# Optimization experiments

Hardware: AMD Instinct MI355X
Metric: run time of the kernel (lower is better)

## Reference

```python
import jax, jax.numpy as jnp
import numpy as np

B, T, M = 32, 14, 2048
Q_DIM, KV_DIM, H = 768, 1024, 12
HD = Q_DIM // H
FF = 4 * Q_DIM
EPS = 1e-5


def layer_norm(x, g, b):
    mu = jnp.mean(x, axis=-1, keepdims=True)
    var = jnp.var(x, axis=-1, keepdims=True)
    return (x - mu) / jnp.sqrt(var + EPS) * g + b


def setup_inputs() -> dict:
    key = jax.random.key(0)
    ks = jax.random.split(key, 12)
    s = 0.02
    return {
        "expert_tokens": jax.random.normal(ks[0], (B, T, Q_DIM), jnp.float32),
        "key_value_embeddings": jax.random.normal(ks[1], (B, M, KV_DIM), jnp.float32),
        # per-expert-token query projections (stacked W_Q_list)
        "WQ": jax.random.normal(ks[2], (T, Q_DIM, Q_DIM), jnp.float32) * s,
        "bQ": jnp.zeros((T, Q_DIM), jnp.float32),
        "WK": jax.random.normal(ks[3], (KV_DIM, Q_DIM), jnp.float32) * s,
        "bK": jnp.zeros((Q_DIM,), jnp.float32),
        "WV": jax.random.normal(ks[4], (KV_DIM, Q_DIM), jnp.float32) * s,
        "bV": jnp.zeros((Q_DIM,), jnp.float32),
        "W1": jax.random.normal(ks[5], (Q_DIM, FF), jnp.float32) * s,
        "b1": jnp.zeros((FF,), jnp.float32),
        "W2": jax.random.normal(ks[6], (FF, Q_DIM), jnp.float32) * s,
        "b2": jnp.zeros((Q_DIM,), jnp.float32),
        "g1": jnp.ones((Q_DIM,), jnp.float32),
        "be1": jnp.zeros((Q_DIM,), jnp.float32),
        "g2": jnp.ones((Q_DIM,), jnp.float32),
        "be2": jnp.zeros((Q_DIM,), jnp.float32),
    }


def reference(expert_tokens, key_value_embeddings, WQ, bQ, WK, bK, WV, bV,
              W1, b1, W2, b2, g1, be1, g2, be2):
    b_, t_, e_ = expert_tokens.shape
    m_ = key_value_embeddings.shape[1]
    # Batched grouped projection: distinct W_Q per expert token (replaces the python loop)
    Q = (jnp.einsum('bte,teq->btq', expert_tokens, WQ) + bQ).reshape(b_, t_, H, HD)
    K = (key_value_embeddings @ WK + bK).reshape(b_, m_, H, HD)
    V = (key_value_embeddings @ WV + bV).reshape(b_, m_, H, HD)
    scale = jnp.sqrt(jnp.asarray(HD, jnp.float32))
    scores = jnp.einsum('bthd,bmhd->bthm', Q, K) / scale
    attn_w = jax.nn.softmax(scores, axis=-1)  # [B,T,H,M]; dropout is identity at eval
    attn_out = jnp.einsum('bthm,bmhd->bthd', attn_w, V).reshape(b_, t_, e_)
    x = layer_norm(expert_tokens + attn_out, g1, be1)
    ff = jnp.maximum(x @ W1 + b1, 0.0) @ W2 + b2
    out = layer_norm(x + ff, g2, be2)
    return out, attn_w
```

## Files before the change

### kernel.cpp

```cpp
#include <hip/hip_runtime.h>
#include <cstdint>
#include <cstddef>

#define BBATCH 32
#define TT 14
#define MM 2048
#define QD 768
#define NHEAD 12
#define HD 64
#define FFD 3072
#define KVD 1024
#define ROWS 448
#define CHSTRIDE 344064

typedef short bf16x8 __attribute__((ext_vector_type(8)));
typedef float f32x4 __attribute__((ext_vector_type(4)));

__device__ __forceinline__ uint16_t f2b(float f) {
  union { float f; uint32_t u; } v; v.f = f;
  uint32_t r = v.u + 0x7fffu + ((v.u >> 16) & 1u);
  return (uint16_t)(r >> 16);
}
__device__ __forceinline__ float b2f(uint16_t b) {
  union { uint32_t u; float f; } v; v.u = ((uint32_t)b) << 16; return v.f;
}

__device__ __forceinline__ void glds16(const void* g, void* l) {
  __builtin_amdgcn_global_load_lds(
      (const __attribute__((address_space(1))) void*)g,
      (__attribute__((address_space(3))) void*)l, 16, 0, 0);
}

__global__ void k_cast8(const float4* __restrict__ in, uint4* __restrict__ out) {
  int i = blockIdx.x * blockDim.x + threadIdx.x;
  float4 a = in[2 * i], b = in[2 * i + 1];
  uint4 o;
  o.x = (uint32_t)f2b(a.x) | ((uint32_t)f2b(a.y) << 16);
  o.y = (uint32_t)f2b(a.z) | ((uint32_t)f2b(a.w) << 16);
  o.z = (uint32_t)f2b(b.x) | ((uint32_t)f2b(b.y) << 16);
  o.w = (uint32_t)f2b(b.z) | ((uint32_t)f2b(b.w) << 16);
  out[i] = o;
}

__global__ void k_transpose_bf16(const float* __restrict__ in, uint16_t* __restrict__ out,
                                 int R, int C) {
  __shared__ float tile[32][33];
  int bz = blockIdx.z;
  int c0 = blockIdx.x * 32, r0 = blockIdx.y * 32;
  int tx = threadIdx.x & 31, ty = threadIdx.x >> 5;
  const float* inb = in + (size_t)bz * R * C;
  uint16_t* outb = out + (size_t)bz * R * C;
#pragma unroll
  for (int rr = 0; rr < 32; rr += 8)
    tile[ty + rr][tx] = inb[(size_t)(r0 + ty + rr) * C + c0 + tx];
  __syncthreads();
#pragma unroll
  for (int rr = 0; rr < 32; rr += 8)
    outb[(size_t)(c0 + ty + rr) * R + r0 + tx] = f2b(tile[tx][ty + rr]);
}

__global__ void k_bias_concat(const float* __restrict__ bK, const float* __restrict__ bV,
                              float* __restrict__ out) {
  int i = blockIdx.x * 256 + threadIdx.x;
  out[i] = (i < QD) ? bK[i] : bV[i - QD];
}

__global__ __launch_bounds__(256, 2) void k_gemm_kv(
    const uint16_t* __restrict__ A, const uint16_t* __restrict__ Bt,
    const float* __restrict__ bias, uint16_t* __restrict__ Kh, uint16_t* __restrict__ Vt) {
  __shared__ __align__(16) uint16_t As[3 * 4096];
  __shared__ __align__(16) uint16_t Bs[3 * 8192];
  const int K = KVD;
  int tid = threadIdx.x;
  int w = tid >> 6, l = tid & 63;

  int wgid = blockIdx.y * 6 + blockIdx.x;
  int swz = (wgid & 7) * 384 + (wgid >> 3);
  int bx = swz % 6, by = swz / 6;
  int m0 = by * 128, n0 = bx * 256;
  int wm = (w >> 1) * 64, wn = (w & 1) * 128;

  f32x4 zero4 = {0.f, 0.f, 0.f, 0.f};
  f32x4 acc[4][8];
#pragma unroll
  for (int i = 0; i < 4; i++)
#pragma unroll
    for (int j = 0; j < 8; j++) acc[i][j] = zero4;

  int sr = tid >> 2;
  int xs8 = (((tid & 3) ^ ((tid >> 3) & 3))) * 8;
  const uint16_t* gA0 = A + (size_t)(m0 + sr) * K + xs8;
  const uint16_t* gA1 = A + (size_t)(m0 + 64 + sr) * K + xs8;
  const uint16_t* gB0 = Bt + (size_t)(n0 + sr) * K + xs8;
  const uint16_t* gB1 = Bt + (size_t)(n0 + 64 + sr) * K + xs8;
  const uint16_t* gB2 = Bt + (size_t)(n0 + 128 + sr) * K + xs8;
  const uint16_t* gB3 = Bt + (size_t)(n0 + 192 + sr) * K + xs8;

  int lm = l & 15, q = l >> 4;
  int qp = (q ^ ((lm >> 1) & 3)) * 8;

  auto stage = [&](int buf, int kt) {
    uint16_t* a = As + buf * 4096 + w * 512;
    uint16_t* b = Bs + buf * 8192 + w * 512;
    glds16(gA0 + kt, a);
    glds16(gA1 + kt, a + 2048);
    glds16(gB0 + kt, b);
    glds16(gB1 + kt, b + 2048);
    glds16(gB2 + kt, b + 4096);
    glds16(gB3 + kt, b + 6144);
  };
  auto compute = [&](int buf) {
    const uint16_t* as = As + buf * 4096;
    const uint16_t* bs = Bs + buf * 8192;
    bf16x8 af[4], bfv[8];
#pragma unroll
    for (int i = 0; i < 4; i++)
      af[i] = *(const bf16x8*)&as[(wm + i * 16 + lm) * 32 + qp];
#pragma unroll
    for (int j = 0; j < 8; j++)
      bfv[j] = *(const bf16x8*)&bs[(wn + j * 16 + lm) * 32 + qp];
#pragma unroll
    for (int i = 0; i < 4; i++)
#pragma unroll
      for (int j = 0; j < 8; j++)
        acc[i][j] = __builtin_amdgcn_mfma_f32_16x16x32_bf16(af[i], bfv[j], acc[i][j], 0, 0, 0);
  };

  const int NT = K / 32;
  stage(0, 0);
  stage(1, 32);
  int cur = 0;
  for (int t = 0; t < NT - 1; ++t) {
    asm volatile("s_waitcnt vmcnt(6)" ::: "memory");
    __builtin_amdgcn_s_barrier();
    if (t + 2 < NT) {
      int sb = cur + 2; if (sb >= 3) sb -= 3;
      stage(sb, (t + 2) * 32);
    }
    compute(cur);
    cur = (cur == 2) ? 0 : cur + 1;
  }
  asm volatile("s_waitcnt vmcnt(0)" ::: "memory");
  __builtin_amdgcn_s_barrier();
  compute(cur);

#pragma unroll
  for (int j = 0; j < 8; j++) {
    int col = n0 + wn + j * 16 + lm;
    float bc = bias[col];
    bool isV = col >= QD;
    int c2 = isV ? col - QD : col;
    int h = c2 >> 6, d = c2 & 63;
#pragma unroll
    for (int i = 0; i < 4; i++) {
      int rowb = m0 + wm + i * 16 + q * 4;
#pragma unroll
      for (int r = 0; r < 4; r++) {
        int row = rowb + r;
        int b = row >> 11, m = row & 2047;
        float v = acc[i][j][r] + bc;
        if (isV)
          Vt[((((size_t)b * NHEAD + h) * HD) + d) * MM + m] = f2b(v);
        else
          Kh[(((size_t)b * NHEAD + h) * MM + m) * HD + d] = f2b(v);
      }
    }
  }
}

template <bool RELU, bool OUTF32>
__global__ __launch_bounds__(256) void k_gemm64(
    const uint16_t* __restrict__ A, const uint16_t* __restrict__ Bt,
    const float* __restrict__ bias, void* __restrict__ Cv, int K, int N) {
  __shared__ __align__(16) uint16_t As[3 * 2048];
  __shared__ __align__(16) uint16_t Bs[3 * 2048];
  int tid = threadIdx.x;
  int w = tid >> 6, l = tid & 63;
  int m0 = blockIdx.y * 64, n0 = blockIdx.x * 64;
  int wm = (w >> 1) * 32, wn = (w & 1) * 32;
  f32x4 zero4 = {0.f, 0.f, 0.f, 0.f};
  f32x4 acc[2][2];
#pragma unroll
  for (int i = 0; i < 2; i++)
#pragma unroll
    for (int j = 0; j < 2; j++) acc[i][j] = zero4;

  int sr = tid >> 2;
  int xs8 = (((tid & 3) ^ ((tid >> 3) & 3))) * 8;
  const uint16_t* gA = A + (size_t)(m0 + sr) * K + xs8;
  const uint16_t* gB = Bt + (size_t)(n0 + sr) * K + xs8;
  int lm = l & 15, q = l >> 4;
  int qp = (q ^ ((lm >> 1) & 3)) * 8;

  auto stage = [&](int buf, int kt) {
    glds16(gA + kt, As + buf * 2048 + w * 512);
    glds16(gB + kt, Bs + buf * 2048 + w * 512);
  };
  auto compute = [&](int buf) {
    const uint16_t* as = As + buf * 2048;
    const uint16_t* bs = Bs + buf * 2048;
    bf16x8 af[2], bfv[2];
#pragma unroll
    for (int i = 0; i < 2; i++) {
      af[i] = *(const bf16x8*)&as[(wm + i * 16 + lm) * 32 + qp];
      bfv[i] = *(const bf16x8*)&bs[(wn + i * 16 + lm) * 32 + qp];
    }
#pragma unroll
    for (int i = 0; i < 2; i++)
#pragma unroll
      for (int j = 0; j < 2; j++)
        acc[i][j] = __builtin_amdgcn_mfma_f32_16x16x32_bf16(af[i], bfv[j], acc[i][j], 0, 0, 0);
  };

  const int NT = K / 32;
  stage(0, 0);
  stage(1, 32);
  int cur = 0;
  for (int t = 0; t < NT - 1; ++t) {
    asm volatile("s_waitcnt vmcnt(2)" ::: "memory");
    __builtin_amdgcn_s_barrier();
    if (t + 2 < NT) {
      int sb = cur + 2; if (sb >= 3) sb -= 3;
      stage(sb, (t + 2) * 32);
    }
    compute(cur);
    cur = (cur == 2) ? 0 : cur + 1;
  }
  asm volatile("s_waitcnt vmcnt(0)" ::: "memory");
  __builtin_amdgcn_s_barrier();
  compute(cur);

#pragma unroll
  for (int j = 0; j < 2; j++) {
    int col = n0 + wn + j * 16 + lm;
    float bc = bias[col];
#pragma unroll
    for (int i = 0; i < 2; i++) {
      int rowb = m0 + wm + i * 16 + q * 4;
#pragma unroll
      for (int r = 0; r < 4; r++) {
        float v = acc[i][j][r] + bc;
        if (RELU) v = fmaxf(v, 0.f);
        if (OUTF32)
          ((float*)Cv)[(size_t)(rowb + r) * N + col] = v;
        else
          ((uint16_t*)Cv)[(size_t)(rowb + r) * N + col] = f2b(v);
      }
    }
  }
}

__global__ __launch_bounds__(256) void k_gemm_q(
    const uint16_t* __restrict__ Xb, const uint16_t* __restrict__ WQt,
    const float* __restrict__ bQ, float* __restrict__ Q) {
  __shared__ __align__(16) uint16_t As[32 * 32];
  __shared__ __align__(16) uint16_t Bs[64 * 32];
  int tid = threadIdx.x;
  int w = tid >> 6, l = tid & 63;
  int t = blockIdx.y, n0 = blockIdx.x * 64;
  const uint16_t* Wt = WQt + (size_t)t * QD * QD;
  f32x4 zero4 = {0.f, 0.f, 0.f, 0.f};
  f32x4 acc[2] = {zero4, zero4};
  int sr = tid >> 2;
  int xs8 = (((tid & 3) ^ ((tid >> 3) & 3))) * 8;
  const uint16_t* gA = Xb + ((size_t)(sr * TT + t)) * QD + xs8;
  const uint16_t* gB = Wt + (size_t)(n0 + sr) * QD + xs8;
  int lm = l & 15, q = l >> 4;
  int qp = (q ^ ((lm >> 1) & 3)) * 8;
  for (int kt = 0; kt < QD; kt += 32) {
    __syncthreads();
    if (tid < 128) glds16(gA + kt, As + w * 512);
    glds16(gB + kt, Bs + w * 512);
    __syncthreads();
    bf16x8 bfv = *(const bf16x8*)&Bs[(w * 16 + lm) * 32 + qp];
#pragma unroll
    for (int i = 0; i < 2; i++) {
      bf16x8 af = *(const bf16x8*)&As[(i * 16 + lm) * 32 + qp];
      acc[i] = __builtin_amdgcn_mfma_f32_16x16x32_bf16(af, bfv, acc[i], 0, 0, 0);
    }
  }
  int col = n0 + w * 16 + lm;
  float bc = bQ[t * QD + col];
#pragma unroll
  for (int i = 0; i < 2; i++) {
    int b0 = i * 16 + q * 4;
#pragma unroll
    for (int r = 0; r < 4; r++) {
      int b = b0 + r;
      Q[((size_t)(b * TT + t)) * QD + col] = acc[i][r] + bc;
    }
  }
}

__global__ __launch_bounds__(256) void k_scores(
    const float* __restrict__ Q,
    const uint16_t* __restrict__ Kh,
    float* __restrict__ AW) {
  __shared__ __align__(16) float Qs[7][64];
  __shared__ float redv[4];
  int tid = threadIdx.x;
  int tg = blockIdx.x, h = blockIdx.y, b = blockIdx.z;
  int t0 = tg * 7;
  for (int i = tid; i < 7 * 64; i += 256) {
    int t = i >> 6, d = i & 63;
    Qs[t][d] = Q[((size_t)(b * TT + t0 + t)) * QD + h * HD + d] * 0.125f;
  }
  __syncthreads();
  float acc[7][8];
#pragma unroll
  for (int t = 0; t < 7; t++)
#pragma unroll
    for (int c = 0; c < 8; c++) acc[t][c] = 0.f;

  const uint16_t* kb = Kh + ((size_t)(b * NHEAD + h)) * MM * HD;
  for (int c = 0; c < 8; c++) {
    const uint16_t* kr = kb + (size_t)(c * 256 + tid) * HD;
#pragma unroll
    for (int dv = 0; dv < 8; dv++) {
      uint4 u = *(const uint4*)(kr + dv * 8);
      float kf[8];
      kf[0] = __uint_as_float(u.x << 16); kf[1] = __uint_as_float(u.x & 0xffff0000u);
      kf[2] = __uint_as_float(u.y << 16); kf[3] = __uint_as_float(u.y & 0xffff0000u);
      kf[4] = __uint_as_float(u.z << 16); kf[5] = __uint_as_float(u.z & 0xffff0000u);
      kf[6] = __uint_as_float(u.w << 16); kf[7] = __uint_as_float(u.w & 0xffff0000u);
#pragma unroll
      for (int t = 0; t < 7; t++) {
        float4 qa = *(const float4*)&Qs[t][dv * 8];
        float4 qb = *(const float4*)&Qs[t][dv * 8 + 4];
        float s = acc[t][c];
        s = fmaf(kf[0], qa.x, s); s = fmaf(kf[1], qa.y, s);
        s = fmaf(kf[2], qa.z, s); s = fmaf(kf[3], qa.w, s);
        s = fmaf(kf[4], qb.x, s); s = fmaf(kf[5], qb.y, s);
        s = fmaf(kf[6], qb.z, s); s = fmaf(kf[7], qb.w, s);
        acc[t][c] = s;
      }
    }
  }
  int lane = tid & 63, w = tid >> 6;
#pragma unroll
  for (int t = 0; t < 7; t++) {
    float mx = acc[t][0];
#pragma unroll
    for (int c = 1; c < 8; c++) mx = fmaxf(mx, acc[t][c]);
#pragma unroll
    for (int o = 32; o > 0; o >>= 1) mx = fmaxf(mx, __shfl_xor(mx, o));
    if (lane == 0) redv[w] = mx;
    __syncthreads();
    mx = fmaxf(fmaxf(redv[0], redv[1]), fmaxf(redv[2], redv[3]));
    __syncthreads();
    float s = 0.f;
#pragma unroll
    for (int c = 0; c < 8; c++) {
      float e = __expf(acc[t][c] - mx);
      acc[t][c] = e;
      s += e;
    }
#pragma unroll
    for (int o = 32; o > 0; o >>= 1) s += __shfl_xor(s, o);
    if (lane == 0) redv[w] = s;
    __syncthreads();
    s = redv[0] + redv[1] + redv[2] + redv[3];
    __syncthreads();
    float inv = 1.f / s;
    size_t rowb = ((size_t)((b * TT + t0 + t) * NHEAD + h)) * MM;
#pragma unroll
    for (int c = 0; c < 8; c++) AW[rowb + c * 256 + tid] = acc[t][c] * inv;
  }
}

__global__ __launch_bounds__(256) void k_attnout(
    const float* __restrict__ AW, const uint16_t* __restrict__ Vt,
    float* __restrict__ pbuf) {
  int tid = threadIdx.x;
  int h = blockIdx.x, b = blockIdx.y, mc = blockIdx.z;
  int d = tid & 63, tg = tid >> 6;
  int m0 = mc * 256;
  const uint16_t* vr = Vt + (((size_t)(b * NHEAD + h)) * HD + d) * MM + m0;
  const float* pb = AW + ((size_t)(b * TT * NHEAD + h)) * MM + m0;
  float acc[4] = {0.f, 0.f, 0.f, 0.f};
#pragma unroll 2
  for (int mcc = 0; mcc < 256; mcc += 8) {
    uint4 u = *(const uint4*)(vr + mcc);
    float vf[8];
    vf[0] = __uint_as_float(u.x << 16); vf[1] = __uint_as_float(u.x & 0xffff0000u);
    vf[2] = __uint_as_float(u.y << 16); vf[3] = __uint_as_float(u.y & 0xffff0000u);
    vf[4] = __uint_as_float(u.z << 16); vf[5] = __uint_as_float(u.z & 0xffff0000u);
    vf[6] = __uint_as_float(u.w << 16); vf[7] = __uint_as_float(u.w & 0xffff0000u);
#pragma unroll
    for (int i = 0; i < 4; i++) {
      int t = tg * 4 + i;
      if (t < TT) {
        const float* pr = pb + (size_t)t * NHEAD * MM + mcc;
        float4 p0 = *(const float4*)pr;
        float4 p1 = *(const float4*)(pr + 4);
        float s = acc[i];
        s = fmaf(vf[0], p0.x, s); s = fmaf(vf[1], p0.y, s);
        s = fmaf(vf[2], p0.z, s); s = fmaf(vf[3], p0.w, s);
        s = fmaf(vf[4], p1.x, s); s = fmaf(vf[5], p1.y, s);
        s = fmaf(vf[6], p1.z, s); s = fmaf(vf[7], p1.w, s);
        acc[i] = s;
      }
    }
  }
#pragma unroll
  for (int i = 0; i < 4; i++) {
    int t = tg * 4 + i;
    if (t < TT)
      pbuf[(size_t)mc * CHSTRIDE + ((size_t)(b * TT + t)) * QD + h * HD + d] = acc[i];
  }
}

template <int NCHUNK>
__global__ __launch_bounds__(256) void k_add_ln(
    const float* __restrict__ X, const float* __restrict__ P,
    const float* __restrict__ g, const float* __restrict__ be,
    float* __restrict__ outF, uint16_t* __restrict__ outB) {
  __shared__ float redS[4], redQ[4];
  int r = blockIdx.x, tid = threadIdx.x;
  size_t base = (size_t)r * QD;
  float e[3];
  float s = 0.f, sq = 0.f;
#pragma unroll
  for (int j = 0; j < 3; j++) {
    int i = tid + j * 256;
    float v = X[base + i];
#pragma unroll
    for (int c = 0; c < NCHUNK; c++) v += P[(size_t)c * CHSTRIDE + base + i];
    e[j] = v; s += v; sq += v * v;
  }
#pragma unroll
  for (int o = 32; o > 0; o >>= 1) { s += __shfl_xor(s, o); sq += __shfl_xor(sq, o); }
  if ((tid & 63) == 0) { redS[tid >> 6] = s; redQ[tid >> 6] = sq; }
  __syncthreads();
  s = redS[0] + redS[1] + redS[2] + redS[3];
  sq = redQ[0] + redQ[1] + redQ[2] + redQ[3];
  float mu = s * (1.f / QD);
  float var = sq * (1.f / QD) - mu * mu;
  float rstd = rsqrtf(var + 1e-5f);
#pragma unroll
  for (int j = 0; j < 3; j++) {
    int i = tid + j * 256;
    float v = (e[j] - mu) * rstd * g[i] + be[i];
    outF[base + i] = v;
    if (outB) outB[base + i] = f2b(v);
  }
}

extern "C" void kernel_launch(void* const* d_in, const int* in_sizes, int n_in,
                              void* d_out, int out_size, void* d_ws, size_t ws_size,
                              hipStream_t stream) {
  const float* tok = (const float*)d_in[0];
  const float* kve = (const float*)d_in[1];
  const float* WQ  = (const float*)d_in[2];
  const float* bQ  = (const float*)d_in[3];
  const float* WK  = (const float*)d_in[4];
  const float* bK  = (const float*)d_in[5];
  const float* WV  = (const float*)d_in[6];
  const float* bV  = (const float*)d_in[7];
  const float* W1  = (const float*)d_in[8];
  const float* b1  = (const float*)d_in[9];
  const float* W2  = (const float*)d_in[10];
  const float* b2  = (const float*)d_in[11];
  const float* g1  = (const float*)d_in[12];
  const float* be1 = (const float*)d_in[13];
  const float* g2  = (const float*)d_in[14];
  const float* be2 = (const float*)d_in[15];

  float* outp = (float*)d_out;
  float* AW = outp + 448 * 768;

  char* p = (char*)d_ws;
  auto nxt = [&](size_t bytes) -> char* {
    char* r = p;
    p += (bytes + 255) & ~(size_t)255;
    return r;
  };
  uint16_t* Abf   = (uint16_t*)nxt((size_t)67108864 * 2);
  uint16_t* Kh    = (uint16_t*)nxt((size_t)50331648 * 2);
  uint16_t* Vt    = (uint16_t*)nxt((size_t)50331648 * 2);
  uint16_t* Wkvt  = (uint16_t*)nxt((size_t)1572864 * 2);
  uint16_t* WQt   = (uint16_t*)nxt((size_t)8257536 * 2);
  uint16_t* W1t   = (uint16_t*)nxt((size_t)2359296 * 2);
  uint16_t* W2t   = (uint16_t*)nxt((size_t)2359296 * 2);
  uint16_t* xtokb = (uint16_t*)nxt((size_t)344064 * 2);
  float* biaskv   = (float*)nxt(1536 * 4);
  float* Qws      = (float*)nxt((size_t)344064 * 4);
  float* pbuf     = (float*)nxt((size_t)8 * CHSTRIDE * 4);
  float* xws      = (float*)nxt((size_t)344064 * 4);
  uint16_t* xbf   = (uint16_t*)nxt((size_t)344064 * 2);
  uint16_t* h1bf  = (uint16_t*)nxt((size_t)1376256 * 2);
  float* yws      = (float*)nxt((size_t)344064 * 4);

  k_cast8<<<dim3(32768), dim3(256), 0, stream>>>((const float4*)kve, (uint4*)Abf);
  k_cast8<<<dim3(168), dim3(256), 0, stream>>>((const float4*)tok, (uint4*)xtokb);
  k_transpose_bf16<<<dim3(24, 32, 1), dim3(256), 0, stream>>>(WK, Wkvt, 1024, 768);
  k_transpose_bf16<<<dim3(24, 32, 1), dim3(256), 0, stream>>>(WV, Wkvt + (size_t)768 * 1024, 1024, 768);
  k_transpose_bf16<<<dim3(24, 24, 14), dim3(256), 0, stream>>>(WQ, WQt, 768, 768);
  k_transpose_bf16<<<dim3(96, 24, 1), dim3(256), 0, stream>>>(W1, W1t, 768, 3072);
  k_transpose_bf16<<<dim3(24, 96, 1), dim3(256), 0, stream>>>(W2, W2t, 3072, 768);
  k_bias_concat<<<dim3(6), dim3(256), 0, stream>>>(bK, bV, biaskv);

  k_gemm_kv<<<dim3(6, 512), dim3(256), 0, stream>>>(Abf, Wkvt, biaskv, Kh, Vt);

  k_gemm_q<<<dim3(12, 14), dim3(256), 0, stream>>>(xtokb, WQt, bQ, Qws);

  k_scores<<<dim3(2, 12, 32), dim3(256), 0, stream>>>(Qws, Kh, AW);

  k_attnout<<<dim3(12, 32, 8), dim3(256), 0, stream>>>(AW, Vt, pbuf);

  k_add_ln<8><<<dim3(448), dim3(256), 0, stream>>>(tok, pbuf, g1, be1, xws, xbf);

  k_gemm64<true, false><<<dim3(48, 7), dim3(256), 0, stream>>>(xbf, W1t, b1, (void*)h1bf, 768, 3072);
  k_gemm64<false, true><<<dim3(12, 7), dim3(256), 0, stream>>>(h1bf, W2t, b2, (void*)yws, 3072, 768);

  k_add_ln<1><<<dim3(448), dim3(256), 0, stream>>>(xws, yws, g2, be2, outp, (uint16_t*)nullptr);
}
```

Before: 1.224 ms.

## Rewrite KV projection GEMM as 256x256 tile with 8 waves and interleaved staging

The KV projection GEMM moves from a 128x256 tile with 4 waves and a 3-stage, 32-wide K pipeline to a 256x256 tile with 8 waves and a 2-buffer, 64-wide K pipeline. Global-to-LDS loads are split into half-tile chunks interleaved between four MFMA phases, separated by barriers, and setprio raises priority during the MFMA bursts. The intent is more data reuse per tile and better overlap of loads with compute in this large GEMM. The cost is more LDS per block (64KB), more barriers, and fewer blocks in the grid.

```diff
diff --git a/kernel.cpp b/kernel.cpp
--- a/kernel.cpp
+++ b/kernel.cpp
@@ -31,6 +31,8 @@
       (__attribute__((address_space(3))) void*)l, 16, 0, 0);
 }
 
+#define BARM asm volatile("s_barrier" ::: "memory")
+
 __global__ void k_cast8(const float4* __restrict__ in, uint4* __restrict__ out) {
   int i = blockIdx.x * blockDim.x + threadIdx.x;
   float4 a = in[2 * i], b = in[2 * i + 1];
@@ -65,95 +67,136 @@
   out[i] = (i < QD) ? bK[i] : bV[i - QD];
 }
 
-__global__ __launch_bounds__(256, 2) void k_gemm_kv(
+__global__ __launch_bounds__(512, 2) void k_gemm_kv(
     const uint16_t* __restrict__ A, const uint16_t* __restrict__ Bt,
     const float* __restrict__ bias, uint16_t* __restrict__ Kh, uint16_t* __restrict__ Vt) {
-  __shared__ __align__(16) uint16_t As[3 * 4096];
-  __shared__ __align__(16) uint16_t Bs[3 * 8192];
+  __shared__ __align__(16) uint16_t As[2 * 16384];
+  __shared__ __align__(16) uint16_t Bs[2 * 16384];
   const int K = KVD;
   int tid = threadIdx.x;
   int w = tid >> 6, l = tid & 63;
+  int wr = w >> 2, wc = w & 3;
 
   int wgid = blockIdx.y * 6 + blockIdx.x;
-  int swz = (wgid & 7) * 384 + (wgid >> 3);
+  int swz = (wgid & 7) * 192 + (wgid >> 3);
   int bx = swz % 6, by = swz / 6;
-  int m0 = by * 128, n0 = bx * 256;
-  int wm = (w >> 1) * 64, wn = (w & 1) * 128;
+  int m0 = by * 256, n0 = bx * 256;
 
   f32x4 zero4 = {0.f, 0.f, 0.f, 0.f};
-  f32x4 acc[4][8];
-#pragma unroll
-  for (int i = 0; i < 4; i++)
-#pragma unroll
-    for (int j = 0; j < 8; j++) acc[i][j] = zero4;
-
-  int sr = tid >> 2;
-  int xs8 = (((tid & 3) ^ ((tid >> 3) & 3))) * 8;
-  const uint16_t* gA0 = A + (size_t)(m0 + sr) * K + xs8;
-  const uint16_t* gA1 = A + (size_t)(m0 + 64 + sr) * K + xs8;
-  const uint16_t* gB0 = Bt + (size_t)(n0 + sr) * K + xs8;
-  const uint16_t* gB1 = Bt + (size_t)(n0 + 64 + sr) * K + xs8;
-  const uint16_t* gB2 = Bt + (size_t)(n0 + 128 + sr) * K + xs8;
-  const uint16_t* gB3 = Bt + (size_t)(n0 + 192 + sr) * K + xs8;
+  f32x4 acc[8][4];
+#pragma unroll
+  for (int i = 0; i < 8; i++)
+#pragma unroll
+    for (int j = 0; j < 4; j++) acc[i][j] = zero4;
+
+  int srow = tid >> 3;
+  int schk8 = ((tid & 7) ^ (srow & 7)) * 8;
+  const uint16_t* gA = A + (size_t)(m0 + srow) * K + schk8;
+  const uint16_t* gB = Bt + (size_t)(n0 + srow) * K + schk8;
+  int ldsW = w * 512;
+
+  auto stA = [&](int b, int T, int half) {
+    uint16_t* d = As + b * 16384 + half * 8192 + ldsW;
+    const uint16_t* s = gA + (size_t)(half * 128) * K + T * 64;
+    glds16(s, d);
+    glds16(s + (size_t)64 * K, d + 4096);
+  };
+  auto stB = [&](int b, int T, int half) {
+    uint16_t* d = Bs + b * 16384 + half * 8192 + ldsW;
+    const uint16_t* s = gB + (size_t)(half * 128) * K + T * 64;
+    glds16(s, d);
+    glds16(s + (size_t)64 * K, d + 4096);
+  };
 
   int lm = l & 15, q = l >> 4;
-  int qp = (q ^ ((lm >> 1) & 3)) * 8;
-
-  auto stage = [&](int buf, int kt) {
-    uint16_t* a = As + buf * 4096 + w * 512;
-    uint16_t* b = Bs + buf * 8192 + w * 512;
-    glds16(gA0 + kt, a);
-    glds16(gA1 + kt, a + 2048);
-    glds16(gB0 + kt, b);
-    glds16(gB1 + kt, b + 2048);
-    glds16(gB2 + kt, b + 4096);
-    glds16(gB3 + kt, b + 6144);
-  };
-  auto compute = [&](int buf) {
-    const uint16_t* as = As + buf * 4096;
-    const uint16_t* bs = Bs + buf * 8192;
-    bf16x8 af[4], bfv[8];
+  int xk = lm & 7;
+  auto LDA = [&](int b, int row, int s) -> bf16x8 {
+    return *(const bf16x8*)&As[b * 16384 + row * 64 + (((s << 2) + q) ^ xk) * 8];
+  };
+  auto LDB = [&](int b, int row, int s) -> bf16x8 {
+    return *(const bf16x8*)&Bs[b * 16384 + row * 64 + (((s << 2) + q) ^ xk) * 8];
+  };
+
+  const int NT = K / 64;
+  stB(0, 0, 0); stB(0, 0, 1); stA(0, 0, 0); stA(0, 0, 1);
+  stB(1, 1, 0);
+  asm volatile("s_waitcnt vmcnt(2)" ::: "memory");
+  BARM;
+
+  int arow = wr * 128 + lm;
+  int brow = wc * 64 + lm;
+
+  for (int t = 0; t < NT; ++t) {
+    int cur = t & 1, nxt = cur ^ 1;
+    bf16x8 a0[4], b0[4], b1[4];
+#pragma unroll
+    for (int i = 0; i < 4; i++) a0[i] = LDA(cur, arow + i * 16, 0);
+#pragma unroll
+    for (int j = 0; j < 4; j++) b0[j] = LDB(cur, brow + j * 16, 0);
+    if (t + 1 < NT) stB(nxt, t + 1, 1);
+    BARM;
+    __builtin_amdgcn_s_setprio(1);
 #pragma unroll
     for (int i = 0; i < 4; i++)
-      af[i] = *(const bf16x8*)&as[(wm + i * 16 + lm) * 32 + qp];
-#pragma unroll
-    for (int j = 0; j < 8; j++)
-      bfv[j] = *(const bf16x8*)&bs[(wn + j * 16 + lm) * 32 + qp];
+#pragma unroll
+      for (int j = 0; j < 4; j++)
+        acc[i][j] = __builtin_amdgcn_mfma_f32_16x16x32_bf16(a0[i], b0[j], acc[i][j], 0, 0, 0);
+    __builtin_amdgcn_s_setprio(0);
+    BARM;
+#pragma unroll
+    for (int i = 0; i < 4; i++) a0[i] = LDA(cur, arow + 64 + i * 16, 0);
+    if (t + 1 < NT) stA(nxt, t + 1, 0);
+    BARM;
+    __builtin_amdgcn_s_setprio(1);
 #pragma unroll
     for (int i = 0; i < 4; i++)
 #pragma unroll
-      for (int j = 0; j < 8; j++)
-        acc[i][j] = __builtin_amdgcn_mfma_f32_16x16x32_bf16(af[i], bfv[j], acc[i][j], 0, 0, 0);
-  };
-
-  const int NT = K / 32;
-  stage(0, 0);
-  stage(1, 32);
-  int cur = 0;
-  for (int t = 0; t < NT - 1; ++t) {
-    asm volatile("s_waitcnt vmcnt(6)" ::: "memory");
-    __builtin_amdgcn_s_barrier();
-    if (t + 2 < NT) {
-      int sb = cur + 2; if (sb >= 3) sb -= 3;
-      stage(sb, (t + 2) * 32);
-    }
-    compute(cur);
-    cur = (cur == 2) ? 0 : cur + 1;
-  }
-  asm volatile("s_waitcnt vmcnt(0)" ::: "memory");
-  __builtin_amdgcn_s_barrier();
-  compute(cur);
-
-#pragma unroll
-  for (int j = 0; j < 8; j++) {
-    int col = n0 + wn + j * 16 + lm;
+      for (int j = 0; j < 4; j++)
+        acc[4 + i][j] = __builtin_amdgcn_mfma_f32_16x16x32_bf16(a0[i], b0[j], acc[4 + i][j], 0, 0, 0);
+    __builtin_amdgcn_s_setprio(0);
+    BARM;
+#pragma unroll
+    for (int i = 0; i < 4; i++) a0[i] = LDA(cur, arow + i * 16, 1);
+#pragma unroll
+    for (int j = 0; j < 4; j++) b1[j] = LDB(cur, brow + j * 16, 1);
+    if (t + 1 < NT) stA(nxt, t + 1, 1);
+    BARM;
+    __builtin_amdgcn_s_setprio(1);
+#pragma unroll
+    for (int i = 0; i < 4; i++)
+#pragma unroll
+      for (int j = 0; j < 4; j++)
+        acc[i][j] = __builtin_amdgcn_mfma_f32_16x16x32_bf16(a0[i], b1[j], acc[i][j], 0, 0, 0);
+    __builtin_amdgcn_s_setprio(0);
+    BARM;
+#pragma unroll
+    for (int i = 0; i < 4; i++) a0[i] = LDA(cur, arow + 64 + i * 16, 1);
+    if (t + 2 < NT) stB(cur, t + 2, 0);
+    BARM;
+    __builtin_amdgcn_s_setprio(1);
+#pragma unroll
+    for (int i = 0; i < 4; i++)
+#pragma unroll
+      for (int j = 0; j < 4; j++)
+        acc[4 + i][j] = __builtin_amdgcn_mfma_f32_16x16x32_bf16(a0[i], b1[j], acc[4 + i][j], 0, 0, 0);
+    __builtin_amdgcn_s_setprio(0);
+    if (t + 2 < NT)
+      asm volatile("s_waitcnt vmcnt(2)" ::: "memory");
+    else if (t + 1 < NT)
+      asm volatile("s_waitcnt vmcnt(0)" ::: "memory");
+    BARM;
+  }
+
+#pragma unroll
+  for (int j = 0; j < 4; j++) {
+    int col = n0 + wc * 64 + j * 16 + lm;
     float bc = bias[col];
     bool isV = col >= QD;
     int c2 = isV ? col - QD : col;
     int h = c2 >> 6, d = c2 & 63;
 #pragma unroll
-    for (int i = 0; i < 4; i++) {
-      int rowb = m0 + wm + i * 16 + q * 4;
+    for (int i = 0; i < 8; i++) {
+      int rowb = m0 + wr * 128 + i * 16 + q * 4;
 #pragma unroll
       for (int r = 0; r < 4; r++) {
         int row = rowb + r;
@@ -500,7 +543,7 @@
   k_transpose_bf16<<<dim3(24, 96, 1), dim3(256), 0, stream>>>(W2, W2t, 3072, 768);
   k_bias_concat<<<dim3(6), dim3(256), 0, stream>>>(bK, bV, biaskv);
 
-  k_gemm_kv<<<dim3(6, 512), dim3(256), 0, stream>>>(Abf, Wkvt, biaskv, Kh, Vt);
+  k_gemm_kv<<<dim3(6, 256), dim3(512), 0, stream>>>(Abf, Wkvt, biaskv, Kh, Vt);
 
   k_gemm_q<<<dim3(12, 14), dim3(256), 0, stream>>>(xtokb, WQt, bQ, Qws);
 
```

Result: no change. 1.219 ms (-0.4%).
